# Kernel optimization log

Measured on AMD Instinct MI355X. Metric: run time of the kernel, lower is better.

The kernel has to match this reference:

```python
import jax, jax.numpy as jnp
import numpy as np

N_HEADS = 2

def setup_inputs() -> dict:
    key = jax.random.key(0)
    ks = jax.random.split(key, 10)
    d, bank, b, t = 192, 1000, 16, 4096
    s = 1.0 / np.sqrt(d)
    return {
        "z": jax.random.normal(ks[0], (b, d, t), jnp.float32),
        "memory_bank": jax.random.normal(ks[1], (d, bank), jnp.float32),
        "Wq": jax.random.normal(ks[2], (d, d), jnp.float32) * s,
        "bq": jax.random.normal(ks[3], (d,), jnp.float32) * 0.02,
        "Wk": jax.random.normal(ks[4], (d, d), jnp.float32) * s,
        "bk": jax.random.normal(ks[5], (d,), jnp.float32) * 0.02,
        "Wv": jax.random.normal(ks[6], (d, d), jnp.float32) * s,
        "bv": jax.random.normal(ks[7], (d,), jnp.float32) * 0.02,
        "Wo": jax.random.normal(ks[8], (d, d), jnp.float32) * s,
        "bo": jax.random.normal(ks[9], (d,), jnp.float32) * 0.02,
    }


def _split_heads(x):
    # x: [b, d, t] -> [b, h, t, dk]  (matches view(b, h, dk, t).transpose(2, 3))
    b, d, t = x.shape
    dk = d // N_HEADS
    return x.reshape(b, N_HEADS, dk, t).transpose(0, 1, 3, 2)


def reference(z, memory_bank, Wq, bq, Wk, bk, Wv, bv, Wo, bo):
    b, d, t = z.shape
    dk = d // N_HEADS
    # memory bank expanded over batch: [b, d, bank]
    c = jnp.broadcast_to(memory_bank[None], (b,) + memory_bank.shape)
    # 1x1 conv projections == per-channel linear
    q = jnp.einsum('oc,bct->bot', Wq, z) + bq[None, :, None]
    k = jnp.einsum('oc,bcs->bos', Wk, c) + bk[None, :, None]
    v = jnp.einsum('oc,bcs->bos', Wv, c) + bv[None, :, None]
    qh = _split_heads(q)  # [b, h, t, dk]
    kh = _split_heads(k)  # [b, h, bank, dk]
    vh = _split_heads(v)  # [b, h, bank, dk]
    scores = jnp.einsum('bhtd,bhsd->bhts', qh, kh) / jnp.sqrt(jnp.asarray(dk, z.dtype))
    p = jax.nn.softmax(scores, axis=-1)  # [b, h, t, bank]
    out = jnp.einsum('bhts,bhsd->bhtd', p, vh)  # [b, h, t, dk]
    out = out.transpose(0, 1, 3, 2).reshape(b, d, t)  # merge heads -> [b, d, t]
    return jnp.einsum('oc,bct->bot', Wo, out) + bo[None, :, None]
```

## Files before the change

### kernel.cpp

```cpp
#include <hip/hip_runtime.h>


typedef float  f32x4  __attribute__((ext_vector_type(4)));
typedef __bf16 bf16;
typedef __bf16 bf16x4 __attribute__((ext_vector_type(4)));
typedef __bf16 bf16x8 __attribute__((ext_vector_type(8)));

#define B_   16
#define D_   192
#define T_   4096
#define BANK 1000
#define SP   1024
#define DK   96
#define SCALE 0.10206207261596577f
#define LOG2E 1.4426950408889634f

__global__ __launch_bounds__(64) void kv_kernel(
    const float* __restrict__ mb, const float* __restrict__ Wk, const float* __restrict__ bk,
    const float* __restrict__ Wv, const float* __restrict__ bv,
    bf16* __restrict__ ktg, bf16* __restrict__ vtg) {
  const int lane = threadIdx.x;
  const int quad = lane >> 4, l15 = lane & 15;
  const int s0 = blockIdx.x * 16;
  const int kvsel = blockIdx.y >> 1, h = blockIdx.y & 1;
  const float* W  = kvsel ? Wv : Wk;
  const float* bs = kvsel ? bv : bk;
  const int s  = s0 + l15;
  const int sc = s < BANK ? s : (BANK - 1);

  f32x4 acc[6];
#pragma unroll
  for (int n = 0; n < 6; ++n) acc[n] = (f32x4){0.f, 0.f, 0.f, 0.f};

  const float* wrow = &W[(size_t)(h * DK + l15) * D_ + quad * 8];
  for (int kb = 0; kb < 6; ++kb) {
    bf16x8 mhi, mlo;
#pragma unroll
    for (int j = 0; j < 8; ++j) {
      float m = mb[(size_t)(kb * 32 + quad * 8 + j) * BANK + sc];
      bf16 hi = (bf16)m;
      mhi[j] = hi;
      mlo[j] = (bf16)(m - (float)hi);
    }
#pragma unroll
    for (int n = 0; n < 6; ++n) {
      const float* wp = wrow + (size_t)n * 16 * D_ + kb * 32;
      f32x4 wa = *(const f32x4*)wp, wb = *(const f32x4*)(wp + 4);
      bf16x8 whi, wlo;
#pragma unroll
      for (int u = 0; u < 4; ++u) {
        bf16 ha = (bf16)wa[u], hb = (bf16)wb[u];
        whi[u] = ha;     wlo[u] = (bf16)(wa[u] - (float)ha);
        whi[4 + u] = hb; wlo[4 + u] = (bf16)(wb[u] - (float)hb);
      }
      acc[n] = __builtin_amdgcn_mfma_f32_16x16x32_bf16(whi, mhi, acc[n], 0, 0, 0);
      acc[n] = __builtin_amdgcn_mfma_f32_16x16x32_bf16(whi, mlo, acc[n], 0, 0, 0);
      acc[n] = __builtin_amdgcn_mfma_f32_16x16x32_bf16(wlo, mhi, acc[n], 0, 0, 0);
    }
  }

  if (kvsel == 0) {
#pragma unroll
    for (int n = 0; n < 6; ++n) {
      f32x4 b4 = *(const f32x4*)&bs[h * DK + n * 16 + quad * 4];
      bf16x4 pk;
#pragma unroll
      for (int r = 0; r < 4; ++r) pk[r] = (bf16)(acc[n][r] + b4[r]);
      *(bf16x4*)&ktg[((size_t)(h * SP + s)) * DK + n * 16 + quad * 4] = pk;
    }
  } else {
#pragma unroll
    for (int n = 0; n < 6; ++n) {
      f32x4 b4 = *(const f32x4*)&bs[h * DK + n * 16 + quad * 4];
#pragma unroll
      for (int r = 0; r < 4; ++r)
        vtg[((size_t)(h * DK + n * 16 + quad * 4 + r)) * SP + s] = (bf16)(acc[n][r] + b4[r]);
    }
  }
}

__global__ __launch_bounds__(256) void proj_kernel(
    const bf16* __restrict__ XT, const float* __restrict__ W,
    const float* __restrict__ bias, float* __restrict__ Y) {
  __shared__ __align__(16) char smem[24576];
  bf16* sB = (bf16*)smem;
  float* sE = (float*)smem;

  const int tid = threadIdx.x;
  const int t0 = blockIdx.x * 256, o0 = blockIdx.y * 64, b = blockIdx.z;
  const int lane = tid & 63, wv = tid >> 6;
  const int quad = lane >> 4, l15 = lane & 15;

  const bf16* ap[4];
#pragma unroll
  for (int m = 0; m < 4; ++m)
    ap[m] = &XT[((size_t)b * T_ + t0 + (wv * 4 + m) * 16 + l15) * D_ + quad * 8];
  bf16x8 acur[4];
#pragma unroll
  for (int m = 0; m < 4; ++m) acur[m] = *(const bf16x8*)ap[m];

#pragma unroll
  for (int r = 0; r < 6; ++r) {
    int g = tid + 256 * r;
    int kb = g >> 8, nt = (g >> 6) & 3, qd = (g >> 4) & 3, l5 = g & 15;
    const float* wp = &W[(o0 + nt * 16 + l5) * D_ + kb * 32 + qd * 8];
    f32x4 wa = *(const f32x4*)wp, wb = *(const f32x4*)(wp + 4);
    bf16x8 pk;
#pragma unroll
    for (int u = 0; u < 4; ++u) { pk[u] = (bf16)wa[u]; pk[4 + u] = (bf16)wb[u]; }
    *(bf16x8*)&sB[(size_t)g * 8] = pk;
  }

  f32x4 acc[4][4];
#pragma unroll
  for (int m = 0; m < 4; ++m)
#pragma unroll
    for (int n = 0; n < 4; ++n) acc[m][n] = (f32x4){0.f, 0.f, 0.f, 0.f};

  __syncthreads();
  for (int kb = 0; kb < 6; ++kb) {
    bf16x8 anext[4];
    if (kb < 5) {
#pragma unroll
      for (int m = 0; m < 4; ++m)
        anext[m] = *(const bf16x8*)(ap[m] + (kb + 1) * 32);
    }
    bf16x8 bf[4];
#pragma unroll
    for (int n = 0; n < 4; ++n)
      bf[n] = *(const bf16x8*)&sB[(size_t)((kb * 4 + n) * 64 + lane) * 8];
#pragma unroll
    for (int m = 0; m < 4; ++m)
#pragma unroll
      for (int n = 0; n < 4; ++n)
        acc[m][n] = __builtin_amdgcn_mfma_f32_16x16x32_bf16(acur[m], bf[n], acc[m][n], 0, 0, 0);
    if (kb < 5) {
#pragma unroll
      for (int m = 0; m < 4; ++m) acur[m] = anext[m];
    }
  }
  __syncthreads();

  float bs[4];
#pragma unroll
  for (int n = 0; n < 4; ++n) bs[n] = bias[o0 + n * 16 + l15];
  float* se = sE + wv * 1088;
#pragma unroll
  for (int m = 0; m < 4; ++m) {
#pragma unroll
    for (int n = 0; n < 4; ++n)
#pragma unroll
      for (int r = 0; r < 4; ++r)
        se[(quad * 4 + r) * 68 + n * 16 + l15] = acc[m][n][r] + bs[n];
#pragma unroll
    for (int p = 0; p < 4; ++p) {
      int o = p * 16 + (lane >> 2), tq = (lane & 3) * 4;
      f32x4 vv;
#pragma unroll
      for (int u = 0; u < 4; ++u) vv[u] = se[(tq + u) * 68 + o];
      *(f32x4*)&Y[((size_t)b * D_ + o0 + o) * T_ + t0 + wv * 64 + m * 16 + tq] = vv;
    }
  }
}

__global__ __launch_bounds__(256) void attn_kernel(
    const float* __restrict__ z, const float* __restrict__ Wq,
    const float* __restrict__ bq, const bf16* __restrict__ ktg,
    const bf16* __restrict__ vtg, bf16* __restrict__ owsT) {
  __shared__ __align__(16) char smem[40960];
  bf16* kt = (bf16*)smem;
  bf16* vt = (bf16*)(smem + 12288);
  bf16* sP = (bf16*)(smem + 24576);
  bf16* qt = (bf16*)smem;

  const int tid = threadIdx.x;
  const int t0 = blockIdx.x * 128, h = blockIdx.y, b = blockIdx.z;
  const int lane = tid & 63, wv = tid >> 6;
  const int quad = lane >> 4, l15 = lane & 15;

  const bf16* kb_g = ktg + (size_t)h * SP * DK;
  const bf16* vb_g = vtg + (size_t)h * DK * SP;
  const bf16* sp_ptr[6];
  int sp_str[6];
#pragma unroll
  for (int r = 0; r < 6; ++r) {
    int g = tid + 256 * r;
    if (g < 768) {
      int kb = g >> 8, n = (g >> 6) & 3, qd = (g >> 4) & 3, l5 = g & 15;
      sp_ptr[r] = kb_g + (size_t)(n * 16 + l5) * DK + kb * 32 + qd * 8;
      sp_str[r] = 64 * DK;
    } else {
      int gv = g - 768, blk = gv >> 6;
      int kbv = blk / 6, n = blk % 6, qd = (gv >> 4) & 3, l5 = gv & 15;
      sp_ptr[r] = vb_g + (size_t)(n * 16 + l5) * SP + kbv * 32 + qd * 8;
      sp_str[r] = 64;
    }
  }
  bf16x8 kreg[6];
#pragma unroll
  for (int r = 0; r < 6; ++r) kreg[r] = *(const bf16x8*)sp_ptr[r];

  f32x4 qacc[2][6];
#pragma unroll
  for (int t2 = 0; t2 < 2; ++t2)
#pragma unroll
    for (int n = 0; n < 6; ++n) qacc[t2][n] = (f32x4){0.f, 0.f, 0.f, 0.f};
  const float* zc0 = &z[((size_t)b * D_ + quad * 8) * T_ + t0 + wv * 32 + l15];
  const float* wrow = &Wq[(size_t)(h * DK + l15) * D_ + quad * 8];
  for (int kb = 0; kb < 6; ++kb) {
    bf16x8 zf[2];
#pragma unroll
    for (int t2 = 0; t2 < 2; ++t2)
#pragma unroll
      for (int j = 0; j < 8; ++j)
        zf[t2][j] = (bf16)zc0[(size_t)(kb * 32 + j) * T_ + t2 * 16];
#pragma unroll
    for (int n = 0; n < 6; ++n) {
      const float* wp = wrow + (size_t)n * 16 * D_ + kb * 32;
      f32x4 wa = *(const f32x4*)wp, wb = *(const f32x4*)(wp + 4);
      bf16x8 wf;
#pragma unroll
      for (int u = 0; u < 4; ++u) { wf[u] = (bf16)wa[u]; wf[4 + u] = (bf16)wb[u]; }
      qacc[0][n] = __builtin_amdgcn_mfma_f32_16x16x32_bf16(wf, zf[0], qacc[0][n], 0, 0, 0);
      qacc[1][n] = __builtin_amdgcn_mfma_f32_16x16x32_bf16(wf, zf[1], qacc[1][n], 0, 0, 0);
    }
  }
#pragma unroll
  for (int t2 = 0; t2 < 2; ++t2)
#pragma unroll
    for (int n = 0; n < 6; ++n) {
      f32x4 bq4 = *(const f32x4*)&bq[h * DK + n * 16 + quad * 4];
      int g = ((n & 1) * 2 + (quad >> 1)) * 16 + l15;
      int gs = g ^ ((g >> 3) & 7);
      bf16x4 pk;
#pragma unroll
      for (int r = 0; r < 4; ++r)
        pk[r] = (bf16)((qacc[t2][n][r] + bq4[r]) * (SCALE * LOG2E));
      *(bf16x4*)&qt[(size_t)(((n >> 1) * 8 + wv * 2 + t2) * 64 + gs) * 8 + (quad & 1) * 4] = pk;
    }
  bf16x8 qf[2][3];
#pragma unroll
  for (int t2 = 0; t2 < 2; ++t2)
#pragma unroll
    for (int kb = 0; kb < 3; ++kb)
      qf[t2][kb] = *(const bf16x8*)&qt[(size_t)((kb * 8 + wv * 2 + t2) * 64 +
                                                (lane ^ ((lane >> 3) & 7))) * 8];

  f32x4 oaccT[2][6];
#pragma unroll
  for (int t2 = 0; t2 < 2; ++t2)
#pragma unroll
    for (int n = 0; n < 6; ++n) oaccT[t2][n] = (f32x4){0.f, 0.f, 0.f, 0.f};
  float m_run[2] = {-1e30f, -1e30f}, l_run[2] = {0.f, 0.f};

  for (int ch = 0; ch < 16; ++ch) {
    __syncthreads();
#pragma unroll
    for (int r = 0; r < 6; ++r)
      *(bf16x8*)(smem + (size_t)(tid + 256 * r) * 16) = kreg[r];
    __syncthreads();
    if (ch < 15) {
#pragma unroll
      for (int r = 0; r < 6; ++r) {
        sp_ptr[r] += sp_str[r];
        kreg[r] = *(const bf16x8*)sp_ptr[r];
      }
    }

    f32x4 scT[2][4];
#pragma unroll
    for (int t2 = 0; t2 < 2; ++t2)
#pragma unroll
      for (int n = 0; n < 4; ++n) scT[t2][n] = (f32x4){0.f, 0.f, 0.f, 0.f};
#pragma unroll
    for (int kb = 0; kb < 3; ++kb) {
#pragma unroll
      for (int n = 0; n < 4; ++n) {
        bf16x8 kf = *(const bf16x8*)&kt[(size_t)((kb * 4 + n) * 64 + lane) * 8];
        scT[0][n] = __builtin_amdgcn_mfma_f32_16x16x32_bf16(kf, qf[0][kb], scT[0][n], 0, 0, 0);
        scT[1][n] = __builtin_amdgcn_mfma_f32_16x16x32_bf16(kf, qf[1][kb], scT[1][n], 0, 0, 0);
      }
    }
    if (ch == 15) {
#pragma unroll
      for (int t2 = 0; t2 < 2; ++t2)
#pragma unroll
        for (int r = 0; r < 4; ++r) {
          scT[t2][3][r] = -1e30f;
          if (quad >= 2) scT[t2][2][r] = -1e30f;
        }
    }

    float mt[2];
#pragma unroll
    for (int t2 = 0; t2 < 2; ++t2) {
      float m8[8];
#pragma unroll
      for (int u = 0; u < 8; ++u)
        m8[u] = fmaxf(scT[t2][u >> 1][(u & 1) * 2], scT[t2][u >> 1][(u & 1) * 2 + 1]);
      float ma = fmaxf(fmaxf(m8[0], m8[1]), fmaxf(m8[2], m8[3]));
      float mb2 = fmaxf(fmaxf(m8[4], m8[5]), fmaxf(m8[6], m8[7]));
      float m0 = fmaxf(ma, mb2);
      m0 = fmaxf(m0, __shfl_xor(m0, 16, 64));
      m0 = fmaxf(m0, __shfl_xor(m0, 32, 64));
      mt[t2] = m0;
    }
    if (!__all(mt[0] - m_run[0] <= 8.f && mt[1] - m_run[1] <= 8.f)) {
#pragma unroll
      for (int t2 = 0; t2 < 2; ++t2) {
        float mn = fmaxf(m_run[t2], mt[t2]);
        float al = exp2f(m_run[t2] - mn);
        m_run[t2] = mn;
        l_run[t2] *= al;
#pragma unroll
        for (int n = 0; n < 6; ++n)
#pragma unroll
          for (int r = 0; r < 4; ++r) oaccT[t2][n][r] *= al;
      }
    }
#pragma unroll
    for (int t2 = 0; t2 < 2; ++t2) {
      float pr[4][4];
#pragma unroll
      for (int n = 0; n < 4; ++n)
#pragma unroll
        for (int r = 0; r < 4; ++r) pr[n][r] = exp2f(scT[t2][n][r] - m_run[t2]);
      float s8[8];
#pragma unroll
      for (int u = 0; u < 8; ++u)
        s8[u] = pr[u >> 1][(u & 1) * 2] + pr[u >> 1][(u & 1) * 2 + 1];
      float ls = ((s8[0] + s8[1]) + (s8[2] + s8[3])) + ((s8[4] + s8[5]) + (s8[6] + s8[7]));
      ls += __shfl_xor(ls, 16, 64);
      ls += __shfl_xor(ls, 32, 64);
      l_run[t2] += ls;
#pragma unroll
      for (int kb2 = 0; kb2 < 2; ++kb2)
#pragma unroll
        for (int nh = 0; nh < 2; ++nh) {
          int n = kb2 * 2 + nh;
          int g = (nh * 2 + (quad >> 1)) * 16 + l15;
          int gs = g ^ ((g >> 3) & 7);
          bf16x4 pk = {(bf16)pr[n][0], (bf16)pr[n][1], (bf16)pr[n][2], (bf16)pr[n][3]};
          *(bf16x4*)&sP[(size_t)(((wv * 2 + t2) * 2 + kb2) * 64 + gs) * 8 +
                        (quad & 1) * 4] = pk;
        }
    }

#pragma unroll
    for (int kb2 = 0; kb2 < 2; ++kb2) {
      bf16x8 pa[2];
#pragma unroll
      for (int t2 = 0; t2 < 2; ++t2)
        pa[t2] = *(const bf16x8*)&sP[(size_t)(((wv * 2 + t2) * 2 + kb2) * 64 +
                                              (lane ^ ((lane >> 3) & 7))) * 8];
#pragma unroll
      for (int n2 = 0; n2 < 6; ++n2) {
        bf16x8 vf = *(const bf16x8*)&vt[(size_t)((kb2 * 6 + n2) * 64 + lane) * 8];
        oaccT[0][n2] = __builtin_amdgcn_mfma_f32_16x16x32_bf16(vf, pa[0], oaccT[0][n2], 0, 0, 0);
        oaccT[1][n2] = __builtin_amdgcn_mfma_f32_16x16x32_bf16(vf, pa[1], oaccT[1][n2], 0, 0, 0);
      }
    }
  }

#pragma unroll
  for (int t2 = 0; t2 < 2; ++t2) {
    float inv = 1.0f / l_run[t2];
    bf16* orow = &owsT[((size_t)b * T_ + t0 + wv * 32 + t2 * 16 + l15) * D_ +
                       h * DK + quad * 4];
#pragma unroll
    for (int n2 = 0; n2 < 6; ++n2) {
      bf16x4 pk = {(bf16)(oaccT[t2][n2][0] * inv), (bf16)(oaccT[t2][n2][1] * inv),
                   (bf16)(oaccT[t2][n2][2] * inv), (bf16)(oaccT[t2][n2][3] * inv)};
      *(bf16x4*)&orow[n2 * 16] = pk;
    }
  }
}

extern "C" void kernel_launch(void* const* d_in, const int* in_sizes, int n_in,
                              void* d_out, int out_size, void* d_ws, size_t ws_size,
                              hipStream_t stream) {
  const float* z  = (const float*)d_in[0];
  const float* mb = (const float*)d_in[1];
  const float* Wq = (const float*)d_in[2];
  const float* bq = (const float*)d_in[3];
  const float* Wk = (const float*)d_in[4];
  const float* bk = (const float*)d_in[5];
  const float* Wv = (const float*)d_in[6];
  const float* bv = (const float*)d_in[7];
  const float* Wo = (const float*)d_in[8];
  const float* bo = (const float*)d_in[9];
  float* out = (float*)d_out;

  bf16* ktg  = (bf16*)d_ws;
  bf16* vtg  = ktg + 2 * SP * DK;
  bf16* owsT = vtg + 2 * DK * SP;

  kv_kernel  <<<dim3(SP / 16, 4),      64,  0, stream>>>(mb, Wk, bk, Wv, bv, ktg, vtg);
  attn_kernel<<<dim3(T_ / 128, 2, B_), 256, 0, stream>>>(z, Wq, bq, ktg, vtg, owsT);
  proj_kernel<<<dim3(T_ / 256, 3, B_), 256, 0, stream>>>(owsT, Wo, bo, out);
}
```

Before: 248.3 us.

## Fuse output projection into attention kernel, loop over both heads per block

Each attention block now processes both heads in sequence for its 128-token tile and keeps the normalized per-head outputs in shared memory. The Wo projection plus bias then runs inside the same kernel, which removes the separate projection kernel and the bf16 workspace round trip through global memory. In exchange the grid is halved (no head dimension), shared memory grows to 64KB per block, which can lower occupancy, and each block reads Wo directly from global memory, converting it to bf16 on the fly. Output stores are per-lane scalar writes of 16 contiguous floats, not the vectorized transposed stores used before.

Result: slower. 334.6 us (+34.7%).

```diff
diff --git a/kernel.cpp b/kernel.cpp
--- a/kernel.cpp
+++ b/kernel.cpp
@@ -79,299 +79,259 @@
   }
 }
 
-__global__ __launch_bounds__(256) void proj_kernel(
-    const bf16* __restrict__ XT, const float* __restrict__ W,
-    const float* __restrict__ bias, float* __restrict__ Y) {
-  __shared__ __align__(16) char smem[24576];
-  bf16* sB = (bf16*)smem;
-  float* sE = (float*)smem;
-
-  const int tid = threadIdx.x;
-  const int t0 = blockIdx.x * 256, o0 = blockIdx.y * 64, b = blockIdx.z;
-  const int lane = tid & 63, wv = tid >> 6;
-  const int quad = lane >> 4, l15 = lane & 15;
-
-  const bf16* ap[4];
-#pragma unroll
-  for (int m = 0; m < 4; ++m)
-    ap[m] = &XT[((size_t)b * T_ + t0 + (wv * 4 + m) * 16 + l15) * D_ + quad * 8];
-  bf16x8 acur[4];
-#pragma unroll
-  for (int m = 0; m < 4; ++m) acur[m] = *(const bf16x8*)ap[m];
-
-#pragma unroll
-  for (int r = 0; r < 6; ++r) {
-    int g = tid + 256 * r;
-    int kb = g >> 8, nt = (g >> 6) & 3, qd = (g >> 4) & 3, l5 = g & 15;
-    const float* wp = &W[(o0 + nt * 16 + l5) * D_ + kb * 32 + qd * 8];
-    f32x4 wa = *(const f32x4*)wp, wb = *(const f32x4*)(wp + 4);
-    bf16x8 pk;
-#pragma unroll
-    for (int u = 0; u < 4; ++u) { pk[u] = (bf16)wa[u]; pk[4 + u] = (bf16)wb[u]; }
-    *(bf16x8*)&sB[(size_t)g * 8] = pk;
-  }
-
-  f32x4 acc[4][4];
-#pragma unroll
-  for (int m = 0; m < 4; ++m)
-#pragma unroll
-    for (int n = 0; n < 4; ++n) acc[m][n] = (f32x4){0.f, 0.f, 0.f, 0.f};
-
-  __syncthreads();
-  for (int kb = 0; kb < 6; ++kb) {
-    bf16x8 anext[4];
-    if (kb < 5) {
-#pragma unroll
-      for (int m = 0; m < 4; ++m)
-        anext[m] = *(const bf16x8*)(ap[m] + (kb + 1) * 32);
-    }
-    bf16x8 bf[4];
-#pragma unroll
-    for (int n = 0; n < 4; ++n)
-      bf[n] = *(const bf16x8*)&sB[(size_t)((kb * 4 + n) * 64 + lane) * 8];
-#pragma unroll
-    for (int m = 0; m < 4; ++m)
-#pragma unroll
-      for (int n = 0; n < 4; ++n)
-        acc[m][n] = __builtin_amdgcn_mfma_f32_16x16x32_bf16(acur[m], bf[n], acc[m][n], 0, 0, 0);
-    if (kb < 5) {
-#pragma unroll
-      for (int m = 0; m < 4; ++m) acur[m] = anext[m];
-    }
-  }
-  __syncthreads();
-
-  float bs[4];
-#pragma unroll
-  for (int n = 0; n < 4; ++n) bs[n] = bias[o0 + n * 16 + l15];
-  float* se = sE + wv * 1088;
-#pragma unroll
-  for (int m = 0; m < 4; ++m) {
-#pragma unroll
-    for (int n = 0; n < 4; ++n)
-#pragma unroll
-      for (int r = 0; r < 4; ++r)
-        se[(quad * 4 + r) * 68 + n * 16 + l15] = acc[m][n][r] + bs[n];
-#pragma unroll
-    for (int p = 0; p < 4; ++p) {
-      int o = p * 16 + (lane >> 2), tq = (lane & 3) * 4;
-      f32x4 vv;
-#pragma unroll
-      for (int u = 0; u < 4; ++u) vv[u] = se[(tq + u) * 68 + o];
-      *(f32x4*)&Y[((size_t)b * D_ + o0 + o) * T_ + t0 + wv * 64 + m * 16 + tq] = vv;
-    }
-  }
-}
-
 __global__ __launch_bounds__(256) void attn_kernel(
     const float* __restrict__ z, const float* __restrict__ Wq,
     const float* __restrict__ bq, const bf16* __restrict__ ktg,
-    const bf16* __restrict__ vtg, bf16* __restrict__ owsT) {
-  __shared__ __align__(16) char smem[40960];
-  bf16* kt = (bf16*)smem;
-  bf16* vt = (bf16*)(smem + 12288);
-  bf16* sP = (bf16*)(smem + 24576);
-  bf16* qt = (bf16*)smem;
+    const bf16* __restrict__ vtg, const float* __restrict__ Wo,
+    const float* __restrict__ bo, float* __restrict__ out) {
+  __shared__ __align__(16) char smem[65536];
+  bf16* kt  = (bf16*)smem;
+  bf16* vt  = (bf16*)(smem + 12288);
+  bf16* sP  = (bf16*)(smem + 24576);
+  bf16* oT0 = (bf16*)(smem + 40960);
+  bf16* oT1 = (bf16*)smem;
+  bf16* qt  = (bf16*)smem;
 
   const int tid = threadIdx.x;
-  const int t0 = blockIdx.x * 128, h = blockIdx.y, b = blockIdx.z;
+  const int t0 = blockIdx.x * 128, b = blockIdx.y;
   const int lane = tid & 63, wv = tid >> 6;
   const int quad = lane >> 4, l15 = lane & 15;
-
-  const bf16* kb_g = ktg + (size_t)h * SP * DK;
-  const bf16* vb_g = vtg + (size_t)h * DK * SP;
-  const bf16* sp_ptr[6];
-  int sp_str[6];
-#pragma unroll
-  for (int r = 0; r < 6; ++r) {
-    int g = tid + 256 * r;
-    if (g < 768) {
-      int kb = g >> 8, n = (g >> 6) & 3, qd = (g >> 4) & 3, l5 = g & 15;
-      sp_ptr[r] = kb_g + (size_t)(n * 16 + l5) * DK + kb * 32 + qd * 8;
-      sp_str[r] = 64 * DK;
-    } else {
-      int gv = g - 768, blk = gv >> 6;
-      int kbv = blk / 6, n = blk % 6, qd = (gv >> 4) & 3, l5 = gv & 15;
-      sp_ptr[r] = vb_g + (size_t)(n * 16 + l5) * SP + kbv * 32 + qd * 8;
-      sp_str[r] = 64;
-    }
-  }
-  bf16x8 kreg[6];
-#pragma unroll
-  for (int r = 0; r < 6; ++r) kreg[r] = *(const bf16x8*)sp_ptr[r];
-
-  f32x4 qacc[2][6];
-#pragma unroll
-  for (int t2 = 0; t2 < 2; ++t2)
-#pragma unroll
-    for (int n = 0; n < 6; ++n) qacc[t2][n] = (f32x4){0.f, 0.f, 0.f, 0.f};
-  const float* zc0 = &z[((size_t)b * D_ + quad * 8) * T_ + t0 + wv * 32 + l15];
-  const float* wrow = &Wq[(size_t)(h * DK + l15) * D_ + quad * 8];
-  for (int kb = 0; kb < 6; ++kb) {
-    bf16x8 zf[2];
-#pragma unroll
-    for (int t2 = 0; t2 < 2; ++t2)
-#pragma unroll
-      for (int j = 0; j < 8; ++j)
-        zf[t2][j] = (bf16)zc0[(size_t)(kb * 32 + j) * T_ + t2 * 16];
-#pragma unroll
-    for (int n = 0; n < 6; ++n) {
-      const float* wp = wrow + (size_t)n * 16 * D_ + kb * 32;
+  const int lsw = lane ^ ((lane >> 3) & 7);
+
+#pragma unroll 1
+  for (int h = 0; h < 2; ++h) {
+    const bf16* kb_g = ktg + (size_t)h * SP * DK;
+    const bf16* vb_g = vtg + (size_t)h * DK * SP;
+    const bf16* sp_ptr[6];
+    int sp_str[6];
+#pragma unroll
+    for (int r = 0; r < 6; ++r) {
+      int g = tid + 256 * r;
+      if (g < 768) {
+        int kb = g >> 8, n = (g >> 6) & 3, qd = (g >> 4) & 3, l5 = g & 15;
+        sp_ptr[r] = kb_g + (size_t)(n * 16 + l5) * DK + kb * 32 + qd * 8;
+        sp_str[r] = 64 * DK;
+      } else {
+        int gv = g - 768, blk = gv >> 6;
+        int kbv = blk / 6, n = blk % 6, qd = (gv >> 4) & 3, l5 = gv & 15;
+        sp_ptr[r] = vb_g + (size_t)(n * 16 + l5) * SP + kbv * 32 + qd * 8;
+        sp_str[r] = 64;
+      }
+    }
+    bf16x8 kreg[6];
+#pragma unroll
+    for (int r = 0; r < 6; ++r) kreg[r] = *(const bf16x8*)sp_ptr[r];
+
+    if (h) __syncthreads();
+
+    f32x4 qacc[2][6];
+#pragma unroll
+    for (int t2 = 0; t2 < 2; ++t2)
+#pragma unroll
+      for (int n = 0; n < 6; ++n) qacc[t2][n] = (f32x4){0.f, 0.f, 0.f, 0.f};
+    const float* zc0 = &z[((size_t)b * D_ + quad * 8) * T_ + t0 + wv * 32 + l15];
+    const float* wrow = &Wq[(size_t)(h * DK + l15) * D_ + quad * 8];
+    for (int kb = 0; kb < 6; ++kb) {
+      bf16x8 zf[2];
+#pragma unroll
+      for (int t2 = 0; t2 < 2; ++t2)
+#pragma unroll
+        for (int j = 0; j < 8; ++j)
+          zf[t2][j] = (bf16)zc0[(size_t)(kb * 32 + j) * T_ + t2 * 16];
+#pragma unroll
+      for (int n = 0; n < 6; ++n) {
+        const float* wp = wrow + (size_t)n * 16 * D_ + kb * 32;
+        f32x4 wa = *(const f32x4*)wp, wb = *(const f32x4*)(wp + 4);
+        bf16x8 wf;
+#pragma unroll
+        for (int u = 0; u < 4; ++u) { wf[u] = (bf16)wa[u]; wf[4 + u] = (bf16)wb[u]; }
+        qacc[0][n] = __builtin_amdgcn_mfma_f32_16x16x32_bf16(wf, zf[0], qacc[0][n], 0, 0, 0);
+        qacc[1][n] = __builtin_amdgcn_mfma_f32_16x16x32_bf16(wf, zf[1], qacc[1][n], 0, 0, 0);
+      }
+    }
+#pragma unroll
+    for (int t2 = 0; t2 < 2; ++t2)
+#pragma unroll
+      for (int n = 0; n < 6; ++n) {
+        f32x4 bq4 = *(const f32x4*)&bq[h * DK + n * 16 + quad * 4];
+        int g = ((n & 1) * 2 + (quad >> 1)) * 16 + l15;
+        int gs = g ^ ((g >> 3) & 7);
+        bf16x4 pk;
+#pragma unroll
+        for (int r = 0; r < 4; ++r)
+          pk[r] = (bf16)((qacc[t2][n][r] + bq4[r]) * (SCALE * LOG2E));
+        *(bf16x4*)&qt[(size_t)(((n >> 1) * 8 + wv * 2 + t2) * 64 + gs) * 8 +
+                      (quad & 1) * 4] = pk;
+      }
+    bf16x8 qf[2][3];
+#pragma unroll
+    for (int t2 = 0; t2 < 2; ++t2)
+#pragma unroll
+      for (int kb = 0; kb < 3; ++kb)
+        qf[t2][kb] = *(const bf16x8*)&qt[(size_t)((kb * 8 + wv * 2 + t2) * 64 + lsw) * 8];
+
+    f32x4 oaccT[2][6];
+#pragma unroll
+    for (int t2 = 0; t2 < 2; ++t2)
+#pragma unroll
+      for (int n = 0; n < 6; ++n) oaccT[t2][n] = (f32x4){0.f, 0.f, 0.f, 0.f};
+    float m_run[2] = {-1e30f, -1e30f}, l_run[2] = {0.f, 0.f};
+
+    for (int ch = 0; ch < 16; ++ch) {
+      __syncthreads();
+#pragma unroll
+      for (int r = 0; r < 6; ++r)
+        *(bf16x8*)(smem + (size_t)(tid + 256 * r) * 16) = kreg[r];
+      __syncthreads();
+      if (ch < 15) {
+#pragma unroll
+        for (int r = 0; r < 6; ++r) {
+          sp_ptr[r] += sp_str[r];
+          kreg[r] = *(const bf16x8*)sp_ptr[r];
+        }
+      }
+
+      f32x4 scT[2][4];
+#pragma unroll
+      for (int t2 = 0; t2 < 2; ++t2)
+#pragma unroll
+        for (int n = 0; n < 4; ++n) scT[t2][n] = (f32x4){0.f, 0.f, 0.f, 0.f};
+#pragma unroll
+      for (int kb = 0; kb < 3; ++kb) {
+#pragma unroll
+        for (int n = 0; n < 4; ++n) {
+          bf16x8 kf = *(const bf16x8*)&kt[(size_t)((kb * 4 + n) * 64 + lane) * 8];
+          scT[0][n] = __builtin_amdgcn_mfma_f32_16x16x32_bf16(kf, qf[0][kb], scT[0][n], 0, 0, 0);
+          scT[1][n] = __builtin_amdgcn_mfma_f32_16x16x32_bf16(kf, qf[1][kb], scT[1][n], 0, 0, 0);
+        }
+      }
+      if (ch == 15) {
+#pragma unroll
+        for (int t2 = 0; t2 < 2; ++t2)
+#pragma unroll
+          for (int r = 0; r < 4; ++r) {
+            scT[t2][3][r] = -1e30f;
+            if (quad >= 2) scT[t2][2][r] = -1e30f;
+          }
+      }
+
+      float mt[2];
+#pragma unroll
+      for (int t2 = 0; t2 < 2; ++t2) {
+        float m8[8];
+#pragma unroll
+        for (int u = 0; u < 8; ++u)
+          m8[u] = fmaxf(scT[t2][u >> 1][(u & 1) * 2], scT[t2][u >> 1][(u & 1) * 2 + 1]);
+        float ma = fmaxf(fmaxf(m8[0], m8[1]), fmaxf(m8[2], m8[3]));
+        float mb2 = fmaxf(fmaxf(m8[4], m8[5]), fmaxf(m8[6], m8[7]));
+        float m0 = fmaxf(ma, mb2);
+        m0 = fmaxf(m0, __shfl_xor(m0, 16, 64));
+        m0 = fmaxf(m0, __shfl_xor(m0, 32, 64));
+        mt[t2] = m0;
+      }
+      if (!__all(mt[0] - m_run[0] <= 8.f && mt[1] - m_run[1] <= 8.f)) {
+#pragma unroll
+        for (int t2 = 0; t2 < 2; ++t2) {
+          float mn = fmaxf(m_run[t2], mt[t2]);
+          float al = exp2f(m_run[t2] - mn);
+          m_run[t2] = mn;
+          l_run[t2] *= al;
+#pragma unroll
+          for (int n = 0; n < 6; ++n)
+#pragma unroll
+            for (int r = 0; r < 4; ++r) oaccT[t2][n][r] *= al;
+        }
+      }
+#pragma unroll
+      for (int t2 = 0; t2 < 2; ++t2) {
+        float pr[4][4];
+#pragma unroll
+        for (int n = 0; n < 4; ++n)
+#pragma unroll
+          for (int r = 0; r < 4; ++r) pr[n][r] = exp2f(scT[t2][n][r] - m_run[t2]);
+        float s8[8];
+#pragma unroll
+        for (int u = 0; u < 8; ++u)
+          s8[u] = pr[u >> 1][(u & 1) * 2] + pr[u >> 1][(u & 1) * 2 + 1];
+        float ls = ((s8[0] + s8[1]) + (s8[2] + s8[3])) + ((s8[4] + s8[5]) + (s8[6] + s8[7]));
+        ls += __shfl_xor(ls, 16, 64);
+        ls += __shfl_xor(ls, 32, 64);
+        l_run[t2] += ls;
+#pragma unroll
+        for (int kb2 = 0; kb2 < 2; ++kb2)
+#pragma unroll
+          for (int nh = 0; nh < 2; ++nh) {
+            int n = kb2 * 2 + nh;
+            int g = (nh * 2 + (quad >> 1)) * 16 + l15;
+            int gs = g ^ ((g >> 3) & 7);
+            bf16x4 pk = {(bf16)pr[n][0], (bf16)pr[n][1], (bf16)pr[n][2], (bf16)pr[n][3]};
+            *(bf16x4*)&sP[(size_t)(((wv * 2 + t2) * 2 + kb2) * 64 + gs) * 8 +
+                          (quad & 1) * 4] = pk;
+          }
+      }
+
+#pragma unroll
+      for (int kb2 = 0; kb2 < 2; ++kb2) {
+        bf16x8 pa[2];
+#pragma unroll
+        for (int t2 = 0; t2 < 2; ++t2)
+          pa[t2] = *(const bf16x8*)&sP[(size_t)(((wv * 2 + t2) * 2 + kb2) * 64 + lsw) * 8];
+#pragma unroll
+        for (int n2 = 0; n2 < 6; ++n2) {
+          bf16x8 vf = *(const bf16x8*)&vt[(size_t)((kb2 * 6 + n2) * 64 + lane) * 8];
+          oaccT[0][n2] = __builtin_amdgcn_mfma_f32_16x16x32_bf16(vf, pa[0], oaccT[0][n2], 0, 0, 0);
+          oaccT[1][n2] = __builtin_amdgcn_mfma_f32_16x16x32_bf16(vf, pa[1], oaccT[1][n2], 0, 0, 0);
+        }
+      }
+    }
+
+    bf16* oTh = h ? oT1 : oT0;
+    if (h) __syncthreads();
+#pragma unroll
+    for (int t2 = 0; t2 < 2; ++t2) {
+      float inv = 1.0f / l_run[t2];
+#pragma unroll
+      for (int n = 0; n < 6; ++n) {
+        int g = ((n & 1) * 2 + (quad >> 1)) * 16 + l15;
+        int gs = g ^ ((g >> 3) & 7);
+        bf16x4 pk;
+#pragma unroll
+        for (int r = 0; r < 4; ++r) pk[r] = (bf16)(oaccT[t2][n][r] * inv);
+        *(bf16x4*)&oTh[(size_t)(((n >> 1) * 8 + wv * 2 + t2) * 64 + gs) * 8 +
+                       (quad & 1) * 4] = pk;
+      }
+    }
+  }
+
+  bf16x8 bfr[2][6];
+#pragma unroll
+  for (int kbo = 0; kbo < 6; ++kbo) {
+    const bf16* src = (kbo < 3) ? oT0 : oT1;
+    int kb = kbo < 3 ? kbo : kbo - 3;
+#pragma unroll
+    for (int t2 = 0; t2 < 2; ++t2)
+      bfr[t2][kbo] = *(const bf16x8*)&src[(size_t)((kb * 8 + wv * 2 + t2) * 64 + lsw) * 8];
+  }
+#pragma unroll
+  for (int n = 0; n < 12; ++n) {
+    f32x4 a0 = (f32x4){0.f, 0.f, 0.f, 0.f}, a1 = (f32x4){0.f, 0.f, 0.f, 0.f};
+    const float* wop = &Wo[(size_t)(n * 16 + l15) * D_ + quad * 8];
+#pragma unroll
+    for (int kbo = 0; kbo < 6; ++kbo) {
+      const float* wp = wop + kbo * 32;
       f32x4 wa = *(const f32x4*)wp, wb = *(const f32x4*)(wp + 4);
       bf16x8 wf;
 #pragma unroll
       for (int u = 0; u < 4; ++u) { wf[u] = (bf16)wa[u]; wf[4 + u] = (bf16)wb[u]; }
-      qacc[0][n] = __builtin_amdgcn_mfma_f32_16x16x32_bf16(wf, zf[0], qacc[0][n], 0, 0, 0);
-      qacc[1][n] = __builtin_amdgcn_mfma_f32_16x16x32_bf16(wf, zf[1], qacc[1][n], 0, 0, 0);
-    }
-  }
-#pragma unroll
-  for (int t2 = 0; t2 < 2; ++t2)
-#pragma unroll
-    for (int n = 0; n < 6; ++n) {
-      f32x4 bq4 = *(const f32x4*)&bq[h * DK + n * 16 + quad * 4];
-      int g = ((n & 1) * 2 + (quad >> 1)) * 16 + l15;
-      int gs = g ^ ((g >> 3) & 7);
-      bf16x4 pk;
-#pragma unroll
-      for (int r = 0; r < 4; ++r)
-        pk[r] = (bf16)((qacc[t2][n][r] + bq4[r]) * (SCALE * LOG2E));
-      *(bf16x4*)&qt[(size_t)(((n >> 1) * 8 + wv * 2 + t2) * 64 + gs) * 8 + (quad & 1) * 4] = pk;
-    }
-  bf16x8 qf[2][3];
-#pragma unroll
-  for (int t2 = 0; t2 < 2; ++t2)
-#pragma unroll
-    for (int kb = 0; kb < 3; ++kb)
-      qf[t2][kb] = *(const bf16x8*)&qt[(size_t)((kb * 8 + wv * 2 + t2) * 64 +
-                                                (lane ^ ((lane >> 3) & 7))) * 8];
-
-  f32x4 oaccT[2][6];
-#pragma unroll
-  for (int t2 = 0; t2 < 2; ++t2)
-#pragma unroll
-    for (int n = 0; n < 6; ++n) oaccT[t2][n] = (f32x4){0.f, 0.f, 0.f, 0.f};
-  float m_run[2] = {-1e30f, -1e30f}, l_run[2] = {0.f, 0.f};
-
-  for (int ch = 0; ch < 16; ++ch) {
-    __syncthreads();
-#pragma unroll
-    for (int r = 0; r < 6; ++r)
-      *(bf16x8*)(smem + (size_t)(tid + 256 * r) * 16) = kreg[r];
-    __syncthreads();
-    if (ch < 15) {
-#pragma unroll
-      for (int r = 0; r < 6; ++r) {
-        sp_ptr[r] += sp_str[r];
-        kreg[r] = *(const bf16x8*)sp_ptr[r];
-      }
-    }
-
-    f32x4 scT[2][4];
-#pragma unroll
-    for (int t2 = 0; t2 < 2; ++t2)
-#pragma unroll
-      for (int n = 0; n < 4; ++n) scT[t2][n] = (f32x4){0.f, 0.f, 0.f, 0.f};
-#pragma unroll
-    for (int kb = 0; kb < 3; ++kb) {
-#pragma unroll
-      for (int n = 0; n < 4; ++n) {
-        bf16x8 kf = *(const bf16x8*)&kt[(size_t)((kb * 4 + n) * 64 + lane) * 8];
-        scT[0][n] = __builtin_amdgcn_mfma_f32_16x16x32_bf16(kf, qf[0][kb], scT[0][n], 0, 0, 0);
-        scT[1][n] = __builtin_amdgcn_mfma_f32_16x16x32_bf16(kf, qf[1][kb], scT[1][n], 0, 0, 0);
-      }
-    }
-    if (ch == 15) {
-#pragma unroll
-      for (int t2 = 0; t2 < 2; ++t2)
-#pragma unroll
-        for (int r = 0; r < 4; ++r) {
-          scT[t2][3][r] = -1e30f;
-          if (quad >= 2) scT[t2][2][r] = -1e30f;
-        }
-    }
-
-    float mt[2];
-#pragma unroll
-    for (int t2 = 0; t2 < 2; ++t2) {
-      float m8[8];
-#pragma unroll
-      for (int u = 0; u < 8; ++u)
-        m8[u] = fmaxf(scT[t2][u >> 1][(u & 1) * 2], scT[t2][u >> 1][(u & 1) * 2 + 1]);
-      float ma = fmaxf(fmaxf(m8[0], m8[1]), fmaxf(m8[2], m8[3]));
-      float mb2 = fmaxf(fmaxf(m8[4], m8[5]), fmaxf(m8[6], m8[7]));
-      float m0 = fmaxf(ma, mb2);
-      m0 = fmaxf(m0, __shfl_xor(m0, 16, 64));
-      m0 = fmaxf(m0, __shfl_xor(m0, 32, 64));
-      mt[t2] = m0;
-    }
-    if (!__all(mt[0] - m_run[0] <= 8.f && mt[1] - m_run[1] <= 8.f)) {
-#pragma unroll
-      for (int t2 = 0; t2 < 2; ++t2) {
-        float mn = fmaxf(m_run[t2], mt[t2]);
-        float al = exp2f(m_run[t2] - mn);
-        m_run[t2] = mn;
-        l_run[t2] *= al;
-#pragma unroll
-        for (int n = 0; n < 6; ++n)
-#pragma unroll
-          for (int r = 0; r < 4; ++r) oaccT[t2][n][r] *= al;
-      }
-    }
-#pragma unroll
-    for (int t2 = 0; t2 < 2; ++t2) {
-      float pr[4][4];
-#pragma unroll
-      for (int n = 0; n < 4; ++n)
-#pragma unroll
-        for (int r = 0; r < 4; ++r) pr[n][r] = exp2f(scT[t2][n][r] - m_run[t2]);
-      float s8[8];
-#pragma unroll
-      for (int u = 0; u < 8; ++u)
-        s8[u] = pr[u >> 1][(u & 1) * 2] + pr[u >> 1][(u & 1) * 2 + 1];
-      float ls = ((s8[0] + s8[1]) + (s8[2] + s8[3])) + ((s8[4] + s8[5]) + (s8[6] + s8[7]));
-      ls += __shfl_xor(ls, 16, 64);
-      ls += __shfl_xor(ls, 32, 64);
-      l_run[t2] += ls;
-#pragma unroll
-      for (int kb2 = 0; kb2 < 2; ++kb2)
-#pragma unroll
-        for (int nh = 0; nh < 2; ++nh) {
-          int n = kb2 * 2 + nh;
-          int g = (nh * 2 + (quad >> 1)) * 16 + l15;
-          int gs = g ^ ((g >> 3) & 7);
-          bf16x4 pk = {(bf16)pr[n][0], (bf16)pr[n][1], (bf16)pr[n][2], (bf16)pr[n][3]};
-          *(bf16x4*)&sP[(size_t)(((wv * 2 + t2) * 2 + kb2) * 64 + gs) * 8 +
-                        (quad & 1) * 4] = pk;
-        }
-    }
-
-#pragma unroll
-    for (int kb2 = 0; kb2 < 2; ++kb2) {
-      bf16x8 pa[2];
-#pragma unroll
-      for (int t2 = 0; t2 < 2; ++t2)
-        pa[t2] = *(const bf16x8*)&sP[(size_t)(((wv * 2 + t2) * 2 + kb2) * 64 +
-                                              (lane ^ ((lane >> 3) & 7))) * 8];
-#pragma unroll
-      for (int n2 = 0; n2 < 6; ++n2) {
-        bf16x8 vf = *(const bf16x8*)&vt[(size_t)((kb2 * 6 + n2) * 64 + lane) * 8];
-        oaccT[0][n2] = __builtin_amdgcn_mfma_f32_16x16x32_bf16(vf, pa[0], oaccT[0][n2], 0, 0, 0);
-        oaccT[1][n2] = __builtin_amdgcn_mfma_f32_16x16x32_bf16(vf, pa[1], oaccT[1][n2], 0, 0, 0);
-      }
-    }
-  }
-
-#pragma unroll
-  for (int t2 = 0; t2 < 2; ++t2) {
-    float inv = 1.0f / l_run[t2];
-    bf16* orow = &owsT[((size_t)b * T_ + t0 + wv * 32 + t2 * 16 + l15) * D_ +
-                       h * DK + quad * 4];
-#pragma unroll
-    for (int n2 = 0; n2 < 6; ++n2) {
-      bf16x4 pk = {(bf16)(oaccT[t2][n2][0] * inv), (bf16)(oaccT[t2][n2][1] * inv),
-                   (bf16)(oaccT[t2][n2][2] * inv), (bf16)(oaccT[t2][n2][3] * inv)};
-      *(bf16x4*)&orow[n2 * 16] = pk;
+      a0 = __builtin_amdgcn_mfma_f32_16x16x32_bf16(wf, bfr[0][kbo], a0, 0, 0, 0);
+      a1 = __builtin_amdgcn_mfma_f32_16x16x32_bf16(wf, bfr[1][kbo], a1, 0, 0, 0);
+    }
+    f32x4 bo4 = *(const f32x4*)&bo[n * 16 + quad * 4];
+#pragma unroll
+    for (int r = 0; r < 4; ++r) {
+      size_t orow = ((size_t)b * D_ + n * 16 + quad * 4 + r) * T_ + t0;
+      out[orow + wv * 32 + l15]      = a0[r] + bo4[r];
+      out[orow + wv * 32 + 16 + l15] = a1[r] + bo4[r];
     }
   }
 }
@@ -391,11 +351,9 @@
   const float* bo = (const float*)d_in[9];
   float* out = (float*)d_out;
 
-  bf16* ktg  = (bf16*)d_ws;
-  bf16* vtg  = ktg + 2 * SP * DK;
-  bf16* owsT = vtg + 2 * DK * SP;
-
-  kv_kernel  <<<dim3(SP / 16, 4),      64,  0, stream>>>(mb, Wk, bk, Wv, bv, ktg, vtg);
-  attn_kernel<<<dim3(T_ / 128, 2, B_), 256, 0, stream>>>(z, Wq, bq, ktg, vtg, owsT);
-  proj_kernel<<<dim3(T_ / 256, 3, B_), 256, 0, stream>>>(owsT, Wo, bo, out);
+  bf16* ktg = (bf16*)d_ws;
+  bf16* vtg = ktg + 2 * SP * DK;
+
+  kv_kernel  <<<dim3(SP / 16, 4),   64,  0, stream>>>(mb, Wk, bk, Wv, bv, ktg, vtg);
+  attn_kernel<<<dim3(T_ / 128, B_), 256, 0, stream>>>(z, Wq, bq, ktg, vtg, Wo, bo, out);
 }
```
